# Performance work log

Hardware: AMD Instinct MI355X
Metric: run time of the kernel (lower is better)

The kernel has to match this reference:

```python
import jax, jax.numpy as jnp
import numpy as np

HEADS = 16
EPS = 1e-5

def _ln(t):
    # LayerNorm over last axis, no affine params
    mu = jnp.mean(t, axis=-1, keepdims=True)
    var = jnp.var(t, axis=-1, keepdims=True)
    return (t - mu) / jnp.sqrt(var + EPS)

def setup_inputs() -> dict:
    key = jax.random.key(0)
    ks = jax.random.split(key, 8)
    b, n, dim, mlp_dim = 4, 2048, 1024, 4096
    s = lambda d: 1.0 / np.sqrt(d)
    return {
        "x": jax.random.normal(ks[0], (b, n, dim), dtype=jnp.float32),
        "Wqkv": jax.random.uniform(ks[1], (dim, 3 * dim), jnp.float32, -s(dim), s(dim)),
        "W1": jax.random.uniform(ks[2], (dim, mlp_dim), jnp.float32, -s(dim), s(dim)),
        "b1": jax.random.uniform(ks[3], (mlp_dim,), jnp.float32, -s(dim), s(dim)),
        "W2": jax.random.uniform(ks[4], (mlp_dim, dim), jnp.float32, -s(mlp_dim), s(mlp_dim)),
        "b2": jax.random.uniform(ks[5], (dim,), jnp.float32, -s(mlp_dim), s(mlp_dim)),
        "Wout": jax.random.uniform(ks[6], (dim, dim), jnp.float32, -s(dim), s(dim)),
        "bout": jax.random.uniform(ks[7], (dim,), jnp.float32, -s(dim), s(dim)),
    }

def reference(x, Wqkv, W1, b1, W2, b2, Wout, bout):
    b, n, dim = x.shape
    h = HEADS
    d = dim // h
    scale = dim ** (-0.5)  # NOTE: module scales by full dim, not head_dim
    qkv = x @ Wqkv  # [b, n, 3*dim]
    qkv = qkv.reshape(b, n, 3, h, d).transpose(2, 0, 3, 1, 4)  # [3, b, h, n, d]
    q, k, v = qkv[0], qkv[1], qkv[2]
    q, k = _ln(q), _ln(k)
    dots = jnp.einsum('bhid,bhjd->bhij', q, k) * scale
    attn = jax.nn.softmax(dots, axis=-1)
    attn_v = jnp.einsum('bhij,bhjd->bhid', attn, v)
    attn_v = attn_v.transpose(0, 2, 1, 3).reshape(b, n, dim)
    attn_out = attn_v @ Wout + bout
    parallel = jax.nn.gelu(x @ W1 + b1, approximate=False) @ W2 + b2
    return _ln(attn_out + parallel)
```

## Files before the change

kernel.cpp:

```cpp
#include <hip/hip_runtime.h>

typedef __attribute__((ext_vector_type(8))) short s16x8;
typedef __attribute__((ext_vector_type(4))) short s16x4;
typedef __attribute__((ext_vector_type(4))) float f32x4;
typedef __attribute__((ext_vector_type(16))) float f32x16;
typedef __attribute__((ext_vector_type(2))) unsigned uint2v;

#define DEVINL __device__ __forceinline__

DEVINL float b2f(short u){ return __uint_as_float(((unsigned)(unsigned short)u) << 16); }
DEVINL short f2bf(float f){
  unsigned u = __float_as_uint(f);
  u += 0x7fffu + ((u >> 16) & 1u);
  return (short)(u >> 16);
}
DEVINL unsigned cvtpk(float lo, float hi){
  unsigned r;
  asm("v_cvt_pk_bf16_f32 %0, %1, %2" : "=v"(r) : "v"(lo), "v"(hi));
  return r;
}
DEVINL float max3f(float a, float b, float c){
  float r; asm("v_max3_f32 %0, %1, %2, %3" : "=v"(r) : "v"(a), "v"(b), "v"(c)); return r;
}

#if __has_builtin(__builtin_amdgcn_exp2f)
#define EXP2F __builtin_amdgcn_exp2f
#else
#define EXP2F exp2f
#endif

DEVINL f32x4 mfma32(s16x8 a, s16x8 b, f32x4 c){
  return __builtin_amdgcn_mfma_f32_16x16x32_bf16(a, b, c, 0, 0, 0);
}
DEVINL f32x16 mfma3216(s16x8 a, s16x8 b, f32x16 c){
  return __builtin_amdgcn_mfma_f32_32x32x16_bf16(a, b, c, 0, 0, 0);
}

DEVINL uint2v pl32swap(unsigned a, unsigned b){
#if __has_builtin(__builtin_amdgcn_permlane32_swap)
  return __builtin_amdgcn_permlane32_swap(a, b, false, false);
#else
  asm volatile("v_permlane32_swap_b32 %0, %1" : "+v"(a), "+v"(b));
  uint2v r; r[0] = a; r[1] = b; return r;
#endif
}

typedef const unsigned __attribute__((address_space(1)))* gas1;
typedef unsigned __attribute__((address_space(3)))* las3;
DEVINL void gload16(const short* g, short* l){
  __builtin_amdgcn_global_load_lds((gas1)g, (las3)l, 16, 0, 0);
}

#define CFENCE asm volatile("" ::: "memory")
#define PBAR  do{ CFENCE; __builtin_amdgcn_sched_barrier(0); __builtin_amdgcn_s_barrier(); \
                  __builtin_amdgcn_sched_barrier(0); CFENCE; }while(0)
#define VMW8 asm volatile("s_waitcnt vmcnt(8)" ::: "memory")
#define VMW4 asm volatile("s_waitcnt vmcnt(4)" ::: "memory")
#define VMW0 asm volatile("s_waitcnt vmcnt(0)" ::: "memory")
#define PRIO1 __builtin_amdgcn_s_setprio(1)
#define PRIO0 __builtin_amdgcn_s_setprio(0)

static const int Bc   = 4;
static const int Nc   = 2048;
static const int DIM  = 1024;
static const int Tc   = Bc * Nc;
static const int MLP  = 4096;
static const int D3   = 3072;

static const size_t OFF_XB    = 0;
static const size_t OFF_WQKVT = OFF_XB    + 16777216;
static const size_t OFF_W1T   = OFF_WQKVT + 6291456;
static const size_t OFF_W2T   = OFF_W1T   + 8388608;
static const size_t OFF_WOUTT = OFF_W2T   + 8388608;
static const size_t OFF_QKV   = OFF_WOUTT + 2097152;
static const size_t OFF_QLN   = OFF_QKV   + 50331648;
static const size_t OFF_KLN   = OFF_QLN   + 16777216;
static const size_t OFF_VT    = OFF_KLN   + 16777216;
static const size_t OFF_ATTNV = OFF_VT    + 16777216;
static const size_t OFF_H     = OFF_QKV;
static const size_t OFF_S2    = OFF_KLN;

__global__ __launch_bounds__(256) void conv_x(const float* __restrict__ x, short* __restrict__ xb){
  size_t i = ((size_t)blockIdx.x * 256 + threadIdx.x) * 8;
  f32x4 v0 = *(const f32x4*)(x + i);
  f32x4 v1 = *(const f32x4*)(x + i + 4);
  s16x8 o;
#pragma unroll
  for (int j = 0; j < 4; ++j){ o[j] = f2bf(v0[j]); o[4+j] = f2bf(v1[j]); }
  *(s16x8*)(xb + i) = o;
}

__global__ __launch_bounds__(256) void transpose_conv(const float* __restrict__ W, short* __restrict__ Wt,
                                                      int K, int N){
  __shared__ float tile[32][33];
  int ntx = N >> 5;
  int tx = blockIdx.x % ntx, ty = blockIdx.x / ntx;
  int r = threadIdx.x >> 3, c = (threadIdx.x & 7) * 4;
  f32x4 v = *(const f32x4*)(W + (size_t)(ty*32 + r)*N + tx*32 + c);
  tile[r][c] = v[0]; tile[r][c+1] = v[1]; tile[r][c+2] = v[2]; tile[r][c+3] = v[3];
  __syncthreads();
  s16x4 o;
#pragma unroll
  for (int j = 0; j < 4; ++j) o[j] = f2bf(tile[c+j][r]);
  *(s16x4*)(Wt + (size_t)(tx*32 + r)*K + ty*32 + c) = o;
}

template<int ACT, int FUSED, int QKVEPI>
__global__ __launch_bounds__(256, 2) void gemmCF(const short* __restrict__ A, const short* __restrict__ A2,
                                                 const short* __restrict__ Bt, const short* __restrict__ Bt2,
                                                 short* __restrict__ C,
                                                 const float* __restrict__ bias, const float* __restrict__ bias2,
                                                 int M, int N, int K1, int K2,
                                                 short* __restrict__ qln, short* __restrict__ kln,
                                                 short* __restrict__ vtb){
  __shared__ short lds[32768];

  const int tid = threadIdx.x;
  const int w = tid >> 6, lane = tid & 63;
  const int lr = lane & 15, g = lane >> 4;
  const int wr = w >> 1, wc = w & 1;
  const int NT1 = K1 >> 6;
  const int NT = NT1 + (FUSED ? (K2 >> 6) : 0);
  const int NIT = NT >> 1;

  const int nbn = N >> 7;
  const int cpx = gridDim.x >> 3;
  const int bid = (int)blockIdx.x;
  const int sw = (bid & 7)*cpx + (bid >> 3);
  const int nbn8 = nbn >> 3;
  const int T8 = sw >> 6, t64 = sw & 63;
  const int bm = (T8 / nbn8)*8 + (t64 >> 3);
  const int bn = (T8 % nbn8)*8 + (t64 & 7);

  const int l2 = lane >> 2;
  const int gsw = ((lane & 3) - ((lane >> 3) & 3)) & 3;
  const int cof = gsw * 8;
  const int qsw8 = ((g + (lr >> 1)) & 3) * 8;

  const short* ap0h = A  + (size_t)(bm*128 + w*16 + l2)*K1 + cof;
  const short* bp0h = Bt + (size_t)(bn*128 + w*16 + l2)*K1 + cof;
  const short* ap0a = FUSED ? (A2  + (size_t)(bm*128 + w*16 + l2)*K2 + cof) : nullptr;
  const short* bp0a = FUSED ? (Bt2 + (size_t)(bn*128 + w*16 + l2)*K2 + cof) : nullptr;

  auto stA = [&](int s, int T_, int kk){
    short* d0 = lds + s*4096 + w*512;
    if (FUSED && T_ >= NT1){
      size_t off = (size_t)(T_ - NT1)*64 + kk*32;
      gload16(ap0a + off, d0);
      gload16(ap0a + (size_t)64*K2 + off, d0 + 2048);
    } else {
      size_t off = (size_t)T_*64 + kk*32;
      gload16(ap0h + off, d0);
      gload16(ap0h + (size_t)64*K1 + off, d0 + 2048);
    }
  };
  auto stB = [&](int s, int T_, int kk){
    short* d0 = lds + 16384 + s*4096 + w*512;
    if (FUSED && T_ >= NT1){
      size_t off = (size_t)(T_ - NT1)*64 + kk*32;
      gload16(bp0a + off, d0);
      gload16(bp0a + (size_t)64*K2 + off, d0 + 2048);
    } else {
      size_t off = (size_t)T_*64 + kk*32;
      gload16(bp0h + off, d0);
      gload16(bp0h + (size_t)64*K1 + off, d0 + 2048);
    }
  };

#define LDA(s, mi) (*(const s16x8*)&lds[(s)*4096 + (wr*64 + (mi)*16 + lr)*32 + qsw8])
#define LDB(s, ni) (*(const s16x8*)&lds[16384 + (s)*4096 + (wc*64 + (ni)*16 + lr)*32 + qsw8])

  f32x4 acc[4][4] = {};
#define MM(ai, r) \
  acc[r][0]=mfma32(ai,b0,acc[r][0]); acc[r][1]=mfma32(ai,b1,acc[r][1]); \
  acc[r][2]=mfma32(ai,b2,acc[r][2]); acc[r][3]=mfma32(ai,b3,acc[r][3]);
#define RD(s) s16x8 a0=LDA(s,0),a1=LDA(s,1),a2=LDA(s,2),a3=LDA(s,3), \
                    b0=LDB(s,0),b1=LDB(s,1),b2=LDB(s,2),b3=LDB(s,3);
#define MM16 MM(a0,0) MM(a1,1) MM(a2,2) MM(a3,3)

  stA(0,0,0); stB(0,0,0);
  stA(1,0,1); stB(1,0,1);
  stA(2,1,0); stB(2,1,0);
  VMW8;
  PBAR;

  for (int i = 0; i < NIT; ++i){
    const int t = i << 1;
    const bool more = (i + 1 < NIT);
    {
      RD(0)
      stA(3, t+1, 1); stB(3, t+1, 1);
      PBAR; PRIO1; MM16 PRIO0;
      VMW8;
      PBAR;
    }
    {
      RD(1)
      if (more){ stA(0, t+2, 0); stB(0, t+2, 0); }
      PBAR; PRIO1; MM16 PRIO0;
      if (more){ VMW8; } else { VMW4; }
      PBAR;
    }
    {
      RD(2)
      if (more){ stA(1, t+2, 1); stB(1, t+2, 1); }
      PBAR; PRIO1; MM16 PRIO0;
      if (more){ VMW8; } else { VMW0; }
      PBAR;
    }
    {
      RD(3)
      if (more){ stA(2, t+3, 0); stB(2, t+3, 0); }
      PBAR; PRIO1; MM16 PRIO0;
      if (more){ VMW8; }
      PBAR;
    }
  }
#undef MM
#undef RD
#undef MM16
#undef LDA
#undef LDB

  if constexpr (QKVEPI){
#pragma unroll
    for (int a = 0; a < 4; ++a){
#pragma unroll
      for (int ni = 0; ni < 4; ++ni){
        const int col = wc*64 + ni*16 + lr;
        f32x4 v = acc[a][ni];
#pragma unroll
        for (int ii = 0; ii < 4; ++ii)
          lds[(wr*64 + a*16 + 4*g + ii)*130 + col] = f2bf(v[ii]);
      }
    }
    __syncthreads();
    const int part = (bn*128) >> 10;
    const int h0 = ((bn*128) & 1023) >> 6;
    const int rg = bm*128;
    const int b = rg >> 11;
    const int tok0 = rg & 2047;

    if (part < 2){
      short* dstbase = part ? kln : qln;
      const float sc = part ? 1.f : 0.04508422003f;
      const int row = tid >> 1, grp = tid & 1;
      const short* src = &lds[row*130 + grp*64];
      float s = 0.f, sq = 0.f;
#pragma unroll
      for (int i2 = 0; i2 < 8; ++i2){
        s16x8 u = *(const s16x8*)(src + i2*8);
#pragma unroll
        for (int j = 0; j < 8; ++j){ float fv = b2f(u[j]); s += fv; sq += fv*fv; }
      }
      const float mu = s * (1.f/64.f);
      const float var = sq * (1.f/64.f) - mu*mu;
      const float inv = rsqrtf(var + 1e-5f) * sc;
      const int bh = b*16 + h0 + grp;
      short* dst = dstbase + ((size_t)bh*Nc + tok0 + row)*64;
#pragma unroll
      for (int i2 = 0; i2 < 8; ++i2){
        s16x8 u = *(const s16x8*)(src + i2*8);
        s16x8 o;
#pragma unroll
        for (int j = 0; j < 8; ++j) o[j] = f2bf((b2f(u[j]) - mu) * inv);
        *(s16x8*)(dst + i2*8) = o;
      }
    } else {
      const int d = tid & 63, hh = (tid >> 6) & 1, half = tid >> 7;
      const int bh = b*16 + h0 + hh;
      short* dst = vtb + ((size_t)bh*64 + d)*Nc + tok0 + half*64;
#pragma unroll
      for (int i2 = 0; i2 < 8; ++i2){
        s16x8 o;
#pragma unroll
        for (int j = 0; j < 8; ++j)
          o[j] = lds[(half*64 + i2*8 + j)*130 + hh*64 + d];
        *(s16x8*)(dst + i2*8) = o;
      }
    }
    return;
  }

#pragma unroll
  for (int a = 0; a < 4; ++a){
#pragma unroll
    for (int ni = 0; ni < 4; ++ni){
      const int col = wc*64 + ni*16 + lr;
      float bv = bias ? bias[bn*128 + col] : 0.f;
      if (FUSED && bias2) bv += bias2[bn*128 + col];
      f32x4 v = acc[a][ni];
#pragma unroll
      for (int ii = 0; ii < 4; ++ii){
        float val = v[ii] + bv;
        if constexpr (ACT) val = 0.5f*val*(1.f + erff(val*0.70710678118f));
        lds[(wr*64 + a*16 + 4*g + ii)*128 + col] = f2bf(val);
      }
    }
  }
  __syncthreads();
  const size_t crow0 = (size_t)bm * 128;
  const int ch = (tid & 15) * 8;
#pragma unroll
  for (int p = 0; p < 8; ++p){
    const int row = p*16 + (tid >> 4);
    *(s16x8*)&C[(crow0 + row)*N + bn*128 + ch] = *(const s16x8*)&lds[row*128 + ch];
  }
}

__global__ __launch_bounds__(256) void attn_kern(const short* __restrict__ qln, const short* __restrict__ kln,
                                                 const short* __restrict__ vtb, short* __restrict__ attnv){
  __shared__ short Ks[2][64*72];
  __shared__ short Vs[2][64*72];
  const int tid = threadIdx.x;
  const int bh = blockIdx.x >> 4, qt = blockIdx.x & 15;
  const int b = bh >> 4, h = bh & 15;
  const int w = tid >> 6, lane = tid & 63;
  const int lq = lane & 31, hi = lane >> 5;
  const int qrow = qt*128 + w*32 + lq;

  const short* qp = qln + ((size_t)bh*Nc + qrow)*64 + hi*8;
  s16x8 qf[4];
#pragma unroll
  for (int m = 0; m < 4; ++m) qf[m] = *(const s16x8*)(qp + m*16);

  f32x16 o0 = {0,0,0,0,0,0,0,0,0,0,0,0,0,0,0,0};
  f32x16 o1 = {0,0,0,0,0,0,0,0,0,0,0,0,0,0,0,0};
  float mrun = -INFINITY, l = 0.f;

  const int sr = tid >> 3;
  const int sc = (tid & 7) * 8;
  const short* kb0 = kln + (size_t)bh*Nc*64;
  const short* vb0 = vtb + (size_t)bh*64*Nc;

  s16x8 kr0, kr1, vr0, vr1;
  {
    kr0 = *(const s16x8*)(kb0 + (size_t)sr*64 + sc);
    kr1 = *(const s16x8*)(kb0 + (size_t)(32 + sr)*64 + sc);
    vr0 = *(const s16x8*)(vb0 + (size_t)sr*Nc + sc);
    vr1 = *(const s16x8*)(vb0 + (size_t)(32 + sr)*Nc + sc);
  }

  for (int kt = 0; kt < 32; ++kt){
    const int cur = kt & 1;
    *(s16x8*)&Ks[cur][sr*72 + sc]        = kr0;
    *(s16x8*)&Ks[cur][(32 + sr)*72 + sc] = kr1;
    *(s16x8*)&Vs[cur][sr*72 + sc]        = vr0;
    *(s16x8*)&Vs[cur][(32 + sr)*72 + sc] = vr1;
    __syncthreads();
    if (kt + 1 < 32){
      const short* kb = kb0 + (size_t)(kt+1)*64*64;
      const short* vb = vb0 + (kt+1)*64;
      kr0 = *(const s16x8*)(kb + (size_t)sr*64 + sc);
      kr1 = *(const s16x8*)(kb + (size_t)(32 + sr)*64 + sc);
      vr0 = *(const s16x8*)(vb + (size_t)sr*Nc + sc);
      vr1 = *(const s16x8*)(vb + (size_t)(32 + sr)*Nc + sc);
    }

    f32x16 st0 = {0,0,0,0,0,0,0,0,0,0,0,0,0,0,0,0};
    f32x16 st1 = {0,0,0,0,0,0,0,0,0,0,0,0,0,0,0,0};
#pragma unroll
    for (int m = 0; m < 4; ++m){
      s16x8 kf0 = *(const s16x8*)&Ks[cur][ lq      *72 + m*16 + hi*8];
      s16x8 kf1 = *(const s16x8*)&Ks[cur][(32 + lq)*72 + m*16 + hi*8];
      st0 = mfma3216(kf0, qf[m], st0);
      st1 = mfma3216(kf1, qf[m], st1);
    }

    float cmax = max3f(st0[0], st0[1], st0[2]);
    cmax = max3f(cmax, st0[3], st0[4]);   cmax = max3f(cmax, st0[5], st0[6]);
    cmax = max3f(cmax, st0[7], st0[8]);   cmax = max3f(cmax, st0[9], st0[10]);
    cmax = max3f(cmax, st0[11], st0[12]); cmax = max3f(cmax, st0[13], st0[14]);
    cmax = max3f(cmax, st0[15], st1[0]);  cmax = max3f(cmax, st1[1], st1[2]);
    cmax = max3f(cmax, st1[3], st1[4]);   cmax = max3f(cmax, st1[5], st1[6]);
    cmax = max3f(cmax, st1[7], st1[8]);   cmax = max3f(cmax, st1[9], st1[10]);
    cmax = max3f(cmax, st1[11], st1[12]); cmax = max3f(cmax, st1[13], st1[14]);
    cmax = fmaxf(cmax, st1[15]);
    cmax = fmaxf(cmax, __shfl_xor(cmax, 32));
    if (__any(cmax > mrun + 8.f)){
      float mnew = fmaxf(mrun, cmax);
      float fr = EXP2F(mrun - mnew);
      l *= fr;
#pragma unroll
      for (int r = 0; r < 16; ++r){ o0[r] *= fr; o1[r] *= fr; }
      mrun = mnew;
    }
    float p0[16], p1[16];
#pragma unroll
    for (int r = 0; r < 16; ++r){
      p0[r] = EXP2F(st0[r] - mrun); l += p0[r];
      p1[r] = EXP2F(st1[r] - mrun); l += p1[r];
    }

#pragma unroll
    for (int kc = 0; kc < 2; ++kc){
      const float* p = kc ? p1 : p0;
#pragma unroll
      for (int kh = 0; kh < 2; ++kh){
        int r0 = kh*8;
        unsigned wa = cvtpk(p[r0+0], p[r0+1]);
        unsigned wb = cvtpk(p[r0+4], p[r0+5]);
        unsigned wc2 = cvtpk(p[r0+2], p[r0+3]);
        unsigned wd = cvtpk(p[r0+6], p[r0+7]);
        uint2v s1 = pl32swap(wa, wb);
        uint2v s2 = pl32swap(wc2, wd);
        union { unsigned u[4]; s16x8 v; } pu;
        pu.u[0] = s1[0]; pu.u[1] = s2[0]; pu.u[2] = s1[1]; pu.u[3] = s2[1];
        s16x8 vf0 = *(const s16x8*)&Vs[cur][ lq      *72 + kc*32 + kh*16 + hi*8];
        s16x8 vf1 = *(const s16x8*)&Vs[cur][(32 + lq)*72 + kc*32 + kh*16 + hi*8];
        o0 = mfma3216(vf0, pu.v, o0);
        o1 = mfma3216(vf1, pu.v, o1);
      }
    }
  }

  l += __shfl_xor(l, 32);
  float inv = 1.f / l;
  short* orow = attnv + ((size_t)(b*Nc + qrow))*DIM + h*64;
#pragma unroll
  for (int r = 0; r < 16; r += 2){
    int dv = (r&3) + 8*(r>>2) + 4*hi;
    *(unsigned*)&orow[dv]      = cvtpk(o0[r]*inv, o0[r+1]*inv);
    *(unsigned*)&orow[32 + dv] = cvtpk(o1[r]*inv, o1[r+1]*inv);
  }
}

__global__ __launch_bounds__(256) void final_ln(const short* __restrict__ s2, float* __restrict__ out){
  __shared__ float red[16];
  int row = blockIdx.x, tid = threadIdx.x;
  size_t base = (size_t)row*DIM + tid*4;
  s16x4 a = *(const s16x4*)(s2 + base);
  float v[4]; float s = 0.f, sq = 0.f;
#pragma unroll
  for (int i = 0; i < 4; ++i){ v[i] = b2f(a[i]); s += v[i]; sq += v[i]*v[i]; }
#pragma unroll
  for (int m = 1; m < 64; m <<= 1){ s += __shfl_xor(s, m); sq += __shfl_xor(sq, m); }
  int wv = tid >> 6;
  if ((tid & 63) == 0){ red[wv] = s; red[8 + wv] = sq; }
  __syncthreads();
  if (tid == 0){
    float S = red[0] + red[1] + red[2] + red[3];
    float Q = red[8] + red[9] + red[10] + red[11];
    float mu = S * (1.f/1024.f);
    float var = Q * (1.f/1024.f) - mu*mu;
    red[12] = mu; red[13] = rsqrtf(var + 1e-5f);
  }
  __syncthreads();
  float mu = red[12], inv = red[13];
#pragma unroll
  for (int i = 0; i < 4; ++i) out[base + i] = (v[i] - mu) * inv;
}

extern "C" void kernel_launch(void* const* d_in, const int* in_sizes, int n_in,
                              void* d_out, int out_size, void* d_ws, size_t ws_size,
                              hipStream_t stream){
  const float* x    = (const float*)d_in[0];
  const float* Wqkv = (const float*)d_in[1];
  const float* W1   = (const float*)d_in[2];
  const float* b1   = (const float*)d_in[3];
  const float* W2   = (const float*)d_in[4];
  const float* b2   = (const float*)d_in[5];
  const float* Wout = (const float*)d_in[6];
  const float* bout = (const float*)d_in[7];
  float* out = (float*)d_out;
  char* ws = (char*)d_ws;

  short* xb    = (short*)(ws + OFF_XB);
  short* wqkvt = (short*)(ws + OFF_WQKVT);
  short* w1t   = (short*)(ws + OFF_W1T);
  short* w2t   = (short*)(ws + OFF_W2T);
  short* woutt = (short*)(ws + OFF_WOUTT);
  short* qln   = (short*)(ws + OFF_QLN);
  short* kln   = (short*)(ws + OFF_KLN);
  short* vtb   = (short*)(ws + OFF_VT);
  short* attnv = (short*)(ws + OFF_ATTNV);
  short* hbuf  = (short*)(ws + OFF_H);
  short* s2    = (short*)(ws + OFF_S2);

  conv_x<<<4096, 256, 0, stream>>>(x, xb);
  transpose_conv<<<(DIM/32)*(D3/32),  256, 0, stream>>>(Wqkv, wqkvt, DIM, D3);
  transpose_conv<<<(DIM/32)*(MLP/32), 256, 0, stream>>>(W1, w1t, DIM, MLP);
  transpose_conv<<<(MLP/32)*(DIM/32), 256, 0, stream>>>(W2, w2t, MLP, DIM);
  transpose_conv<<<(DIM/32)*(DIM/32), 256, 0, stream>>>(Wout, woutt, DIM, DIM);

  gemmCF<0,0,1><<<(Tc/128)*(D3/128), 256, 0, stream>>>(xb, xb, wqkvt, wqkvt, nullptr,
                                                       nullptr, nullptr, Tc, D3, DIM, DIM,
                                                       qln, kln, vtb);
  attn_kern<<<64*16, 256, 0, stream>>>(qln, kln, vtb, attnv);

  gemmCF<1,0,0><<<(Tc/128)*(MLP/128), 256, 0, stream>>>(xb, xb, w1t, w1t, hbuf,
                                                        b1, nullptr, Tc, MLP, DIM, DIM,
                                                        nullptr, nullptr, nullptr);
  gemmCF<0,1,0><<<(Tc/128)*(DIM/128), 256, 0, stream>>>(hbuf, attnv, w2t, woutt, s2,
                                                        b2, bout, Tc, DIM, MLP, DIM,
                                                        nullptr, nullptr, nullptr);

  final_ln<<<Tc, 256, 0, stream>>>(s2, out);
}
```

Before: 414.1 us.

## Switch GEMM to 3-stage ring buffer and raise occupancy to 3 blocks

Replaces the 4-stage, unrolled-by-4 LDS pipeline in the bf16 GEMM with a 3-stage rotating ring buffer. Each stage holds one 32-wide K slice of A and B, which shrinks shared memory from 64KB to 48KB. Launch bounds go from 2 to 3 blocks per CU to hide latency with more resident waves. The cost is a shallower prefetch distance, index rotation inside the loop, and tighter register limits that could cause spills.

```diff
diff --git a/kernel.cpp b/kernel.cpp
--- a/kernel.cpp
+++ b/kernel.cpp
@@ -54,7 +54,6 @@
 #define CFENCE asm volatile("" ::: "memory")
 #define PBAR  do{ CFENCE; __builtin_amdgcn_sched_barrier(0); __builtin_amdgcn_s_barrier(); \
                   __builtin_amdgcn_sched_barrier(0); CFENCE; }while(0)
-#define VMW8 asm volatile("s_waitcnt vmcnt(8)" ::: "memory")
 #define VMW4 asm volatile("s_waitcnt vmcnt(4)" ::: "memory")
 #define VMW0 asm volatile("s_waitcnt vmcnt(0)" ::: "memory")
 #define PRIO1 __builtin_amdgcn_s_setprio(1)
@@ -106,22 +105,21 @@
 }
 
 template<int ACT, int FUSED, int QKVEPI>
-__global__ __launch_bounds__(256, 2) void gemmCF(const short* __restrict__ A, const short* __restrict__ A2,
+__global__ __launch_bounds__(256, 3) void gemmCF(const short* __restrict__ A, const short* __restrict__ A2,
                                                  const short* __restrict__ Bt, const short* __restrict__ Bt2,
                                                  short* __restrict__ C,
                                                  const float* __restrict__ bias, const float* __restrict__ bias2,
                                                  int M, int N, int K1, int K2,
                                                  short* __restrict__ qln, short* __restrict__ kln,
                                                  short* __restrict__ vtb){
-  __shared__ short lds[32768];
+  __shared__ short lds[24576];
 
   const int tid = threadIdx.x;
   const int w = tid >> 6, lane = tid & 63;
   const int lr = lane & 15, g = lane >> 4;
   const int wr = w >> 1, wc = w & 1;
-  const int NT1 = K1 >> 6;
-  const int NT = NT1 + (FUSED ? (K2 >> 6) : 0);
-  const int NIT = NT >> 1;
+  const int NP1 = K1 >> 5;
+  const int NP = NP1 + (FUSED ? (K2 >> 5) : 0);
 
   const int nbn = N >> 7;
   const int cpx = gridDim.x >> 3;
@@ -142,83 +140,55 @@
   const short* ap0a = FUSED ? (A2  + (size_t)(bm*128 + w*16 + l2)*K2 + cof) : nullptr;
   const short* bp0a = FUSED ? (Bt2 + (size_t)(bn*128 + w*16 + l2)*K2 + cof) : nullptr;
 
-  auto stA = [&](int s, int T_, int kk){
-    short* d0 = lds + s*4096 + w*512;
-    if (FUSED && T_ >= NT1){
-      size_t off = (size_t)(T_ - NT1)*64 + kk*32;
-      gload16(ap0a + off, d0);
-      gload16(ap0a + (size_t)64*K2 + off, d0 + 2048);
+  auto stage = [&](int s, int p){
+    short* da = lds + s*4096 + w*512;
+    short* db = lds + 12288 + s*4096 + w*512;
+    if (FUSED && p >= NP1){
+      size_t off = (size_t)(p - NP1)*32;
+      gload16(ap0a + off, da);
+      gload16(ap0a + (size_t)64*K2 + off, da + 2048);
+      gload16(bp0a + off, db);
+      gload16(bp0a + (size_t)64*K2 + off, db + 2048);
     } else {
-      size_t off = (size_t)T_*64 + kk*32;
-      gload16(ap0h + off, d0);
-      gload16(ap0h + (size_t)64*K1 + off, d0 + 2048);
+      size_t off = (size_t)p*32;
+      gload16(ap0h + off, da);
+      gload16(ap0h + (size_t)64*K1 + off, da + 2048);
+      gload16(bp0h + off, db);
+      gload16(bp0h + (size_t)64*K1 + off, db + 2048);
     }
   };
-  auto stB = [&](int s, int T_, int kk){
-    short* d0 = lds + 16384 + s*4096 + w*512;
-    if (FUSED && T_ >= NT1){
-      size_t off = (size_t)(T_ - NT1)*64 + kk*32;
-      gload16(bp0a + off, d0);
-      gload16(bp0a + (size_t)64*K2 + off, d0 + 2048);
-    } else {
-      size_t off = (size_t)T_*64 + kk*32;
-      gload16(bp0h + off, d0);
-      gload16(bp0h + (size_t)64*K1 + off, d0 + 2048);
-    }
-  };
 
 #define LDA(s, mi) (*(const s16x8*)&lds[(s)*4096 + (wr*64 + (mi)*16 + lr)*32 + qsw8])
-#define LDB(s, ni) (*(const s16x8*)&lds[16384 + (s)*4096 + (wc*64 + (ni)*16 + lr)*32 + qsw8])
+#define LDB(s, ni) (*(const s16x8*)&lds[12288 + (s)*4096 + (wc*64 + (ni)*16 + lr)*32 + qsw8])
 
   f32x4 acc[4][4] = {};
-#define MM(ai, r) \
-  acc[r][0]=mfma32(ai,b0,acc[r][0]); acc[r][1]=mfma32(ai,b1,acc[r][1]); \
-  acc[r][2]=mfma32(ai,b2,acc[r][2]); acc[r][3]=mfma32(ai,b3,acc[r][3]);
-#define RD(s) s16x8 a0=LDA(s,0),a1=LDA(s,1),a2=LDA(s,2),a3=LDA(s,3), \
-                    b0=LDB(s,0),b1=LDB(s,1),b2=LDB(s,2),b3=LDB(s,3);
-#define MM16 MM(a0,0) MM(a1,1) MM(a2,2) MM(a3,3)
-
-  stA(0,0,0); stB(0,0,0);
-  stA(1,0,1); stB(1,0,1);
-  stA(2,1,0); stB(2,1,0);
-  VMW8;
+
+  stage(0, 0);
+  stage(1, 1);
+  VMW4;
   PBAR;
 
-  for (int i = 0; i < NIT; ++i){
-    const int t = i << 1;
-    const bool more = (i + 1 < NIT);
-    {
-      RD(0)
-      stA(3, t+1, 1); stB(3, t+1, 1);
-      PBAR; PRIO1; MM16 PRIO0;
-      VMW8;
-      PBAR;
-    }
-    {
-      RD(1)
-      if (more){ stA(0, t+2, 0); stB(0, t+2, 0); }
-      PBAR; PRIO1; MM16 PRIO0;
-      if (more){ VMW8; } else { VMW4; }
-      PBAR;
-    }
-    {
-      RD(2)
-      if (more){ stA(1, t+2, 1); stB(1, t+2, 1); }
-      PBAR; PRIO1; MM16 PRIO0;
-      if (more){ VMW8; } else { VMW0; }
-      PBAR;
-    }
-    {
-      RD(3)
-      if (more){ stA(2, t+3, 0); stB(2, t+3, 0); }
-      PBAR; PRIO1; MM16 PRIO0;
-      if (more){ VMW8; }
-      PBAR;
-    }
-  }
-#undef MM
-#undef RD
-#undef MM16
+  int sA = 0, sB = 1, sC = 2;
+  for (int p = 0; p < NP; ++p){
+    s16x8 a0=LDA(sA,0), a1=LDA(sA,1), a2=LDA(sA,2), a3=LDA(sA,3);
+    s16x8 b0=LDB(sA,0), b1=LDB(sA,1), b2=LDB(sA,2), b3=LDB(sA,3);
+    const bool st = (p + 2 < NP);
+    if (st) stage(sC, p + 2);
+    PBAR;
+    PRIO1;
+    acc[0][0]=mfma32(a0,b0,acc[0][0]); acc[0][1]=mfma32(a0,b1,acc[0][1]);
+    acc[0][2]=mfma32(a0,b2,acc[0][2]); acc[0][3]=mfma32(a0,b3,acc[0][3]);
+    acc[1][0]=mfma32(a1,b0,acc[1][0]); acc[1][1]=mfma32(a1,b1,acc[1][1]);
+    acc[1][2]=mfma32(a1,b2,acc[1][2]); acc[1][3]=mfma32(a1,b3,acc[1][3]);
+    acc[2][0]=mfma32(a2,b0,acc[2][0]); acc[2][1]=mfma32(a2,b1,acc[2][1]);
+    acc[2][2]=mfma32(a2,b2,acc[2][2]); acc[2][3]=mfma32(a2,b3,acc[2][3]);
+    acc[3][0]=mfma32(a3,b0,acc[3][0]); acc[3][1]=mfma32(a3,b1,acc[3][1]);
+    acc[3][2]=mfma32(a3,b2,acc[3][2]); acc[3][3]=mfma32(a3,b3,acc[3][3]);
+    PRIO0;
+    if (st){ VMW4; } else if (p + 1 < NP){ VMW0; }
+    PBAR;
+    int t = sA; sA = sB; sB = sC; sC = t;
+  }
 #undef LDA
 #undef LDB
 
```

Result: slower. 573.4 us (+38.5%).
